# Kernel optimization log

Measured on AMD Instinct MI355X. Metric: run time of the kernel, lower is better.

Reference implementation:

```python
import jax, jax.numpy as jnp
import numpy as np

B, T, U, H, M, K, C = 64, 800, 80, 512, 20, 10, 80  # batch, tsteps, char len, rnn_size, nmixtures, kmixtures, char_vec_len


def _lstm(x, W, Uw, b):
    """Keras-semantics LSTM (gate order i,f,g,o), zero initial state. x: [B,T,D] -> [B,T,H]."""
    xg = jnp.einsum('btd,dh->bth', x, W) + b  # precompute input contribution
    h0 = jnp.zeros((x.shape[0], Uw.shape[0]), x.dtype)
    c0 = jnp.zeros_like(h0)

    def step(carry, zt):
        h, c = carry
        z = zt + h @ Uw
        i, f, g, o = jnp.split(z, 4, axis=-1)
        c = jax.nn.sigmoid(f) * c + jax.nn.sigmoid(i) * jnp.tanh(g)
        h = jax.nn.sigmoid(o) * jnp.tanh(c)
        return (h, c), h

    _, hs = jax.lax.scan(step, (h0, c0), jnp.swapaxes(xg, 0, 1))
    return jnp.swapaxes(hs, 0, 1)


def _forward(stroke_data, char_seq, kappa0, W0, U0, b0, W1, U1, b1, W2, U2, b2, Wa, ba, Wm, bm):
    lstm0_out = _lstm(stroke_data, W0, U0, b0)  # [B,T,H]
    # Attention window: the per-timestep loop in the source only carries kappa,
    # which is a running sum of exp(kappa_offset) -> vectorize via cumsum.
    abk = jnp.exp(jnp.einsum('bth,hk->btk', lstm0_out, Wa) + ba)  # [B,T,3K]
    alpha, beta, koff = jnpp_split = jnp.split(abk, 3, axis=-1)
    kappa = kappa0[:, None, :, 0] + jnp.cumsum(koff, axis=1)  # [B,T,K]
    u = jnp.arange(char_seq.shape[1], dtype=stroke_data.dtype)  # [U]
    # phi: [B,T,U] = sum_k alpha * exp(-beta * (kappa - u)^2)
    phi = jnp.sum(alpha[..., None] * jnp.exp(-beta[..., None] * (kappa[..., None] - u) ** 2), axis=2)
    windows = jnp.einsum('btu,buc->btc', phi, char_seq)  # [B,T,C]
    aug = jnp.concatenate([lstm0_out, windows, stroke_data], axis=-1)
    lstm1_out = _lstm(aug, W1, U1, b1)
    lstm2_out = _lstm(lstm1_out, W2, U2, b2)
    mdn = jnp.einsum('bth,hn->btn', lstm2_out, Wm) + bm  # [B,T,1+6M]
    eos_hat = mdn[..., 0:1]
    pi_hat, mu1, mu2, s1_hat, s2_hat, rho_hat = jnp.split(mdn[..., 1:], 6, axis=-1)
    return jnp.concatenate([
        jax.nn.sigmoid(-eos_hat),
        jax.nn.softmax(pi_hat, axis=-1),
        mu1, mu2,
        jnp.exp(s1_hat), jnp.exp(s2_hat),
        jnp.tanh(rho_hat),
    ], axis=-1)  # [B,T,1+6M]


def setup_inputs() -> dict:
    key = jax.random.key(0)
    ks = jax.random.split(key, 12)
    init = lambda k, shape: jax.random.truncated_normal(k, -2.0, 2.0, shape, jnp.float32) * 0.075
    return {
        'stroke_data': jax.random.normal(ks[0], (B, T, 3), jnp.float32),
        'char_seq': jax.nn.one_hot(jax.random.randint(ks[1], (B, U), 0, C), C, dtype=jnp.float32),
        'kappa0': jnp.zeros((B, K, 1), jnp.float32),
        'W0': init(ks[2], (3, 4 * H)), 'U0': init(ks[3], (H, 4 * H)), 'b0': jnp.zeros((4 * H,)),
        'W1': init(ks[4], (H + C + 3, 4 * H)), 'U1': init(ks[5], (H, 4 * H)), 'b1': jnp.zeros((4 * H,)),
        'W2': init(ks[6], (H, 4 * H)), 'U2': init(ks[7], (H, 4 * H)), 'b2': jnp.zeros((4 * H,)),
        'Wa': init(ks[8], (H, 3 * K)),
        'ba': -3.0 + 0.25 * jax.random.truncated_normal(ks[9], -2.0, 2.0, (3 * K,), jnp.float32),
        'Wm': init(ks[10], (H, 1 + 6 * M)), 'bm': jnp.zeros((1 + 6 * M,)),
    }


def reference(stroke_data, char_seq, kappa0, W0, U0, b0, W1, U1, b1, W2, U2, b2, Wa, ba, Wm, bm):
    return _forward(stroke_data, char_seq, kappa0, W0, U0, b0, W1, U1, b1, W2, U2, b2, Wa, ba, Wm, bm)
```

## Files before the change

### kernel.cpp

```cpp
#include <hip/hip_runtime.h>

typedef unsigned short u16;
typedef unsigned int u32;
typedef short v8s __attribute__((ext_vector_type(8)));
typedef float v4f __attribute__((ext_vector_type(4)));
typedef unsigned int v4u __attribute__((ext_vector_type(4)));
typedef unsigned int v2u __attribute__((ext_vector_type(2)));

#define MFMA16 __builtin_amdgcn_mfma_f32_16x16x32_bf16

constexpr int TT = 800;
constexpr int NBLK = 178;

constexpr int AUGB  = 2240;
constexpr int AUG2B = 2048;

constexpr size_t AUGR_OFF  = 131072;
constexpr size_t AUG2R_OFF = AUGR_OFF + (size_t)4 * 64 * AUGB;
constexpr size_t WAT_OFF   = AUG2R_OFF + (size_t)4 * 64 * AUG2B;
constexpr size_t WS_ZERO   = WAT_OFF + (size_t)32 * 512 * 2;

constexpr u32 SMEM_BYTES = 82944;

enum { G_S0D = 0, G_SAD = 1, G_S1D = 2, G_S2D = 3, G_S1R = 4, G_SAR = 5, G_S2R = 6, G_SMR = 7 };

__device__ __forceinline__ float bf2f(u16 u) { return __uint_as_float(((u32)u) << 16); }
__device__ __forceinline__ u16 f2bf(float f) {
    u32 x = __float_as_uint(f);
    return (u16)((x + 0x7fffu + ((x >> 16) & 1u)) >> 16);
}
__device__ __forceinline__ short f2bfs(float f) { return (short)f2bf(f); }
__device__ __forceinline__ float sigf(float x) { return 1.f / (1.f + __expf(-x)); }
__device__ __forceinline__ float tanhf2(float x) { return 1.f - 2.f / (1.f + __expf(2.f * x)); }

__device__ __forceinline__ __amdgpu_buffer_rsrc_t mkrsrc(const void* p) {
    return __builtin_amdgcn_make_buffer_rsrc((void*)p, (short)0, -1, 0x00020000);
}
__device__ __forceinline__ v4u ldu4(__amdgpu_buffer_rsrc_t r, int off) {
    return __builtin_amdgcn_raw_buffer_load_b128(r, off, 0, 17);
}
__device__ __forceinline__ v2u ldu8(__amdgpu_buffer_rsrc_t r, int off) {
    return __builtin_amdgcn_raw_buffer_load_b64(r, off, 0, 17);
}
__device__ __forceinline__ void stq8(__amdgpu_buffer_rsrc_t r, int off, u16 a, u16 b, u16 c, u16 d) {
    v2u t; t[0] = (u32)a | ((u32)b << 16); t[1] = (u32)c | ((u32)d << 16);
    __builtin_amdgcn_raw_buffer_store_b64(t, r, off, 0, 17);
}
__device__ __forceinline__ void stq4(__amdgpu_buffer_rsrc_t r, int off, u16 a, u16 b) {
    u32 t = (u32)a | ((u32)b << 16);
    __builtin_amdgcn_raw_buffer_store_b32(t, r, off, 0, 17);
}

__device__ __forceinline__ void publish(u32* ctrl, int g, int t, int sub) {
    __hip_atomic_fetch_add(ctrl + g * 4096 + (t & 3) * 1024 + (sub & 15) * 64, 1u,
                           __ATOMIC_RELAXED, __HIP_MEMORY_SCOPE_AGENT);
}
__device__ __forceinline__ void wait4(u32* ctrl,
    int g0, int t0, u32 n0, int m0, int g1, int t1, u32 n1, int m1,
    int g2, int t2, u32 n2, int m2, int g3, int t3, u32 n3, int m3)
{
    if (threadIdx.x < 64) {
        const int lane = threadIdx.x;
        const int cl = lane >> 4, k = lane & 15;
        int g, tt, mb; u32 nn;
        if (cl == 0)      { g = g0; tt = t0; nn = n0; mb = m0; }
        else if (cl == 1) { g = g1; tt = t1; nn = n1; mb = m1; }
        else if (cl == 2) { g = g2; tt = t2; nn = n2; mb = m2; }
        else              { g = g3; tt = t3; nn = n3; mb = m3; }
        const u32 tgt = (g >= 0 && tt >= 0) ? nn * (u32)((tt >> 2) + 1) : 0u;
        u32* p = (tgt > 0) ? (ctrl + g * 4096 + (tt & 3) * 1024 + (mb + (k & 7)) * 64) : (u32*)0;
        int sp = 0;
        for (;;) {
            u32 v = p ? __hip_atomic_load(p, __ATOMIC_RELAXED, __HIP_MEMORY_SCOPE_AGENT) : 0u;
            v += __shfl_xor(v, 1); v += __shfl_xor(v, 2);
            v += __shfl_xor(v, 4); v += __shfl_xor(v, 8);
            const bool bad = (tgt > 0) && (v < tgt);
            if (__ballot(bad) == 0ull) break;
            if (sp >= 2) __builtin_amdgcn_s_sleep(4);
            else if (sp == 1) __builtin_amdgcn_s_sleep(1);
            sp++;
        }
    }
    __syncthreads();
}

__global__ void wat_init(const float* __restrict__ Wa, u16* __restrict__ WaT) {
    __amdgpu_buffer_rsrc_t r = mkrsrc(WaT);
    for (int idx = blockIdx.x * 256 + threadIdx.x; idx < 32 * 512 / 2; idx += gridDim.x * 256) {
        const int e0 = idx * 2, e1 = e0 + 1;
        const int n0 = e0 >> 9, k0 = e0 & 511;
        const int n1 = e1 >> 9, k1 = e1 & 511;
        const u16 a = (n0 < 30) ? f2bf(Wa[k0 * 30 + n0]) : (u16)0;
        const u16 b = (n1 < 30) ? f2bf(Wa[k1 * 30 + n1]) : (u16)0;
        stq4(r, idx * 4, a, b);
    }
}

__global__ __launch_bounds__(256, 1) void hw_main(
    const float* __restrict__ stroke, const float* __restrict__ charseq, const float* __restrict__ kappa0,
    const float* __restrict__ W0, const float* __restrict__ U0, const float* __restrict__ b0,
    const float* __restrict__ W1, const float* __restrict__ U1, const float* __restrict__ b1,
    const float* __restrict__ W2, const float* __restrict__ U2, const float* __restrict__ b2,
    const float* __restrict__ ba, const float* __restrict__ Wm, const float* __restrict__ bm,
    float* __restrict__ out, char* __restrict__ ws)
{
    extern __shared__ __align__(16) char smem[];
    u32* ctrl = (u32*)ws;
    u16* augr  = (u16*)(ws + AUGR_OFF);
    u16* aug2r = (u16*)(ws + AUG2R_OFF);
    const u16* WaT = (const u16*)(ws + WAT_OFF);

    const int blk = blockIdx.x, tid = threadIdx.x;
    const int wave = tid >> 6, lane = tid & 63;
    const int quad = lane >> 4, l15 = lane & 15;

    if (blk < 32) {
        const int cs = blk & 15, mg = blk >> 4;
        const int mb = mg * 8, sub = mb + (cs & 7);
        __amdgpu_buffer_rsrc_t ra = mkrsrc(augr);
        u16*   aL  = (u16*)smem;
        float* zb  = (float*)(smem + 33280);
        float* w0s = (float*)(smem + 50176);
        float* b0s = (float*)(smem + 51712);
        if (tid < 128) {
            const int cn2 = (tid >> 5) * 512 + cs * 32 + (tid & 31);
            b0s[tid] = b0[cn2];
            #pragma unroll
            for (int d = 0; d < 3; d++) w0s[d * 128 + tid] = W0[d * 2048 + cn2];
        }
        v8s bw0[16], bw1[16];
        {
            const int cnA = wave * 512 + cs * 32 + l15;
            const int cnB = cnA + 16;
            #pragma unroll
            for (int kc = 0; kc < 16; kc++)
                #pragma unroll
                for (int j = 0; j < 8; j++) {
                    const int k = kc * 32 + quad * 8 + j;
                    bw0[kc][j] = f2bfs(U0[k * 2048 + cnA]);
                    bw1[kc][j] = f2bfs(U0[k * 2048 + cnB]);
                }
        }
        float cst[4] = {0.f, 0.f, 0.f, 0.f};
        const int bl_ = tid & 31;
        const int bpre = mg * 32 + bl_;
        __syncthreads();
        #pragma unroll 1
        for (int t = 0; t < TT; t++) {
            const float xx0 = stroke[(bpre * TT + t) * 3 + 0];
            const float xx1 = stroke[(bpre * TT + t) * 3 + 1];
            const float xx2 = stroke[(bpre * TT + t) * 3 + 2];
            wait4(ctrl, G_S0D, t - 1, 32, mb, G_S1R, t - 4, 64, mb, G_SAR, t - 4, 16, mb, -1, 0, 0, 0);
            {
                const int base = (((t + 3) & 3) * 64 + mg * 32) * AUGB;
                #pragma unroll
                for (int c8 = 0; c8 < 8; c8++) {
                    const int c = tid + 256 * c8;
                    const int row = c >> 6, off = c & 63;
                    v4u d = ldu4(ra, base + row * AUGB + off * 16);
                    *(v4u*)((char*)aL + row * 1040 + off * 16) = d;
                }
            }
            __syncthreads();
            v4f c0a = {0,0,0,0}, c0b = {0,0,0,0}, c1a = {0,0,0,0}, c1b = {0,0,0,0};
            const int xo = quad * 16;
            #pragma unroll
            for (int kc = 0; kc < 16; kc++) {
                v8s x0 = *(const v8s*)((const char*)aL + l15 * 1040 + kc * 64 + xo);
                v8s x1 = *(const v8s*)((const char*)aL + (16 + l15) * 1040 + kc * 64 + xo);
                c0a = MFMA16(x0, bw0[kc], c0a, 0, 0, 0);
                c1a = MFMA16(x0, bw1[kc], c1a, 0, 0, 0);
                c0b = MFMA16(x1, bw0[kc], c0b, 0, 0, 0);
                c1b = MFMA16(x1, bw1[kc], c1b, 0, 0, 0);
            }
            const int n0 = wave * 32 + l15, n1 = n0 + 16;
            #pragma unroll
            for (int r = 0; r < 4; r++) {
                zb[(quad * 4 + r) * 132 + n0] = c0a[r];
                zb[(quad * 4 + r) * 132 + n1] = c1a[r];
                zb[(16 + quad * 4 + r) * 132 + n0] = c0b[r];
                zb[(16 + quad * 4 + r) * 132 + n1] = c1b[r];
            }
            __syncthreads();
            {
                const int bl = tid & 31, jj = tid >> 5;
                const int b = mg * 32 + bl;
                u16 hv[4];
                #pragma unroll
                for (int m = 0; m < 4; m++) {
                    const int j = jj * 4 + m;
                    float z[4];
                    #pragma unroll
                    for (int g = 0; g < 4; g++) {
                        const int n = g * 32 + j;
                        z[g] = zb[bl * 132 + n] + b0s[n] + xx0 * w0s[n] + xx1 * w0s[128 + n] + xx2 * w0s[256 + n];
                    }
                    const float cc = sigf(z[1]) * cst[m] + sigf(z[0]) * tanhf2(z[2]);
                    cst[m] = cc;
                    hv[m] = f2bf(sigf(z[3]) * tanhf2(cc));
                }
                stq8(ra, ((t & 3) * 64 + b) * AUGB + (cs * 32 + jj * 4) * 2, hv[0], hv[1], hv[2], hv[3]);
            }
            __syncthreads();
            if (tid == 0) publish(ctrl, G_S0D, t, sub);
        }
    } else if (blk < 96) {
        const int q = blk - 32, cs = q >> 1, mg = q & 1;
        const int mb = mg * 8, sub = mb + (cs & 7);
        __amdgpu_buffer_rsrc_t ra = mkrsrc(augr);
        __amdgpu_buffer_rsrc_t r2 = mkrsrc(aug2r);
        u16*   aL  = (u16*)smem;
        float* zb  = (float*)(smem + 72192);
        float* b1s = (float*)(smem + 80896);
        if (tid < 64) b1s[tid] = b1[(tid >> 4) * 512 + cs * 16 + (tid & 15)];
        v8s bw[35];
        {
            const int cn = wave * 512 + cs * 16 + l15;
            #pragma unroll
            for (int kc = 0; kc < 35; kc++)
                #pragma unroll
                for (int j = 0; j < 8; j++) {
                    const int k = kc * 32 + quad * 8 + j;
                    short v = 0;
                    if (k < 595) v = f2bfs(W1[k * 2048 + cn]);
                    else if (k >= 596 && k < 1108) v = f2bfs(U1[(k - 596) * 2048 + cn]);
                    bw[kc][j] = v;
                }
        }
        if (tid < 32) { v4u z4 = {0,0,0,0}; *(v4u*)((char*)aL + tid * 2256 + 2224) = z4; }
        float cst[2] = {0.f, 0.f};
        __syncthreads();
        #pragma unroll 1
        for (int t = 0; t < TT; t++) {
            wait4(ctrl, G_S0D, t, 32, mb, G_SAD, t, 16, mb, G_S2R, t - 4, 64, mb, -1, 0, 0, 0);
            {
                const int base = ((t & 3) * 64 + mg * 32) * AUGB;
                #pragma unroll
                for (int c10 = 0; c10 < 10; c10++) {
                    const int c = tid + 256 * c10;
                    if (c < 2400) {
                        const int row = c / 75, off = c - row * 75;
                        v4u d = ldu4(ra, base + row * AUGB + off * 16);
                        *(v4u*)((char*)aL + row * 2256 + off * 16) = d;
                    }
                }
            }
            __syncthreads();
            if (tid == 0) publish(ctrl, G_S1R, t, sub);
            wait4(ctrl, G_S1D, t - 1, 64, mb, -1, 0, 0, 0, -1, 0, 0, 0, -1, 0, 0, 0);
            {
                const int base = ((t & 3) * 64 + mg * 32) * AUGB;
                if (tid < 32) {
                    v2u d8 = ldu8(ra, base + tid * AUGB + 1192);
                    *(v2u*)((char*)aL + tid * 2256 + 1192) = d8;
                }
                #pragma unroll
                for (int c8 = 0; c8 < 8; c8++) {
                    const int c = tid + 256 * c8;
                    const int row = c >> 6, off = 75 + (c & 63);
                    v4u d = ldu4(ra, base + row * AUGB + off * 16);
                    *(v4u*)((char*)aL + row * 2256 + off * 16) = d;
                }
            }
            v4f c0 = {0,0,0,0}, c1 = {0,0,0,0};
            const int xo = quad * 16;
            #pragma unroll
            for (int kc = 0; kc < 18; kc++) {
                v8s x0 = *(const v8s*)((const char*)aL + l15 * 2256 + kc * 64 + xo);
                v8s x1 = *(const v8s*)((const char*)aL + (16 + l15) * 2256 + kc * 64 + xo);
                c0 = MFMA16(x0, bw[kc], c0, 0, 0, 0);
                c1 = MFMA16(x1, bw[kc], c1, 0, 0, 0);
            }
            __syncthreads();
            #pragma unroll
            for (int kc = 18; kc < 35; kc++) {
                v8s x0 = *(const v8s*)((const char*)aL + l15 * 2256 + kc * 64 + xo);
                v8s x1 = *(const v8s*)((const char*)aL + (16 + l15) * 2256 + kc * 64 + xo);
                c0 = MFMA16(x0, bw[kc], c0, 0, 0, 0);
                c1 = MFMA16(x1, bw[kc], c1, 0, 0, 0);
            }
            #pragma unroll
            for (int r = 0; r < 4; r++) {
                zb[(quad * 4 + r) * 68 + wave * 17 + l15] = c0[r];
                zb[(16 + quad * 4 + r) * 68 + wave * 17 + l15] = c1[r];
            }
            __syncthreads();
            {
                const int bl = tid & 31, jj = tid >> 5;
                const int b = mg * 32 + bl;
                u16 hv[2];
                #pragma unroll
                for (int m = 0; m < 2; m++) {
                    const int j = jj * 2 + m;
                    float z[4];
                    #pragma unroll
                    for (int g = 0; g < 4; g++)
                        z[g] = zb[bl * 68 + g * 17 + j] + b1s[g * 16 + j];
                    const float cc = sigf(z[1]) * cst[m] + sigf(z[0]) * tanhf2(z[2]);
                    cst[m] = cc;
                    hv[m] = f2bf(sigf(z[3]) * tanhf2(cc));
                }
                stq4(ra, (((t + 1) & 3) * 64 + b) * AUGB + (596 + cs * 16 + jj * 2) * 2, hv[0], hv[1]);
                stq4(r2, ((t & 3) * 64 + b) * AUG2B + (cs * 16 + jj * 2) * 2, hv[0], hv[1]);
            }
            __syncthreads();
            if (tid == 0) publish(ctrl, G_S1D, t, sub);
        }
    } else if (blk < 160) {
        const int q = blk - 96, cs = q >> 1, mg = q & 1;
        const int mb = mg * 8, sub = mb + (cs & 7);
        __amdgpu_buffer_rsrc_t r2 = mkrsrc(aug2r);
        u16*   aL  = (u16*)smem;
        float* zb  = (float*)(smem + 66048);
        float* b2s = (float*)(smem + 74752);
        if (tid < 64) b2s[tid] = b2[(tid >> 4) * 512 + cs * 16 + (tid & 15)];
        v8s bw[32];
        {
            const int cn = wave * 512 + cs * 16 + l15;
            #pragma unroll
            for (int kc = 0; kc < 32; kc++)
                #pragma unroll
                for (int j = 0; j < 8; j++) {
                    const int k = kc * 32 + quad * 8 + j;
                    bw[kc][j] = (k < 512) ? f2bfs(W2[k * 2048 + cn]) : f2bfs(U2[(k - 512) * 2048 + cn]);
                }
        }
        float cst[2] = {0.f, 0.f};
        __syncthreads();
        #pragma unroll 1
        for (int t = 0; t < TT; t++) {
            wait4(ctrl, G_S1D, t, 64, mb, G_SMR, t - 4, 2, mb, -1, 0, 0, 0, -1, 0, 0, 0);
            {
                const int base = ((t & 3) * 64 + mg * 32) * AUG2B;
                #pragma unroll
                for (int c8 = 0; c8 < 8; c8++) {
                    const int c = tid + 256 * c8;
                    const int row = c >> 6, off = c & 63;
                    v4u d = ldu4(r2, base + row * AUG2B + off * 16);
                    *(v4u*)((char*)aL + row * 2064 + off * 16) = d;
                }
            }
            __syncthreads();
            if (tid == 0) publish(ctrl, G_S2R, t, sub);
            wait4(ctrl, G_S2D, t - 1, 64, mb, -1, 0, 0, 0, -1, 0, 0, 0, -1, 0, 0, 0);
            {
                const int base = ((t & 3) * 64 + mg * 32) * AUG2B;
                #pragma unroll
                for (int c8 = 0; c8 < 8; c8++) {
                    const int c = tid + 256 * c8;
                    const int row = c >> 6, off = 64 + (c & 63);
                    v4u d = ldu4(r2, base + row * AUG2B + off * 16);
                    *(v4u*)((char*)aL + row * 2064 + off * 16) = d;
                }
            }
            v4f c0 = {0,0,0,0}, c1 = {0,0,0,0};
            const int xo = quad * 16;
            #pragma unroll
            for (int kc = 0; kc < 16; kc++) {
                v8s x0 = *(const v8s*)((const char*)aL + l15 * 2064 + kc * 64 + xo);
                v8s x1 = *(const v8s*)((const char*)aL + (16 + l15) * 2064 + kc * 64 + xo);
                c0 = MFMA16(x0, bw[kc], c0, 0, 0, 0);
                c1 = MFMA16(x1, bw[kc], c1, 0, 0, 0);
            }
            __syncthreads();
            #pragma unroll
            for (int kc = 16; kc < 32; kc++) {
                v8s x0 = *(const v8s*)((const char*)aL + l15 * 2064 + kc * 64 + xo);
                v8s x1 = *(const v8s*)((const char*)aL + (16 + l15) * 2064 + kc * 64 + xo);
                c0 = MFMA16(x0, bw[kc], c0, 0, 0, 0);
                c1 = MFMA16(x1, bw[kc], c1, 0, 0, 0);
            }
            #pragma unroll
            for (int r = 0; r < 4; r++) {
                zb[(quad * 4 + r) * 68 + wave * 17 + l15] = c0[r];
                zb[(16 + quad * 4 + r) * 68 + wave * 17 + l15] = c1[r];
            }
            __syncthreads();
            {
                const int bl = tid & 31, jj = tid >> 5;
                const int b = mg * 32 + bl;
                u16 hv[2];
                #pragma unroll
                for (int m = 0; m < 2; m++) {
                    const int j = jj * 2 + m;
                    float z[4];
                    #pragma unroll
                    for (int g = 0; g < 4; g++)
                        z[g] = zb[bl * 68 + g * 17 + j] + b2s[g * 16 + j];
                    const float cc = sigf(z[1]) * cst[m] + sigf(z[0]) * tanhf2(z[2]);
                    cst[m] = cc;
                    hv[m] = f2bf(sigf(z[3]) * tanhf2(cc));
                }
                stq4(r2, (((t + 1) & 3) * 64 + b) * AUG2B + (512 + cs * 16 + jj * 2) * 2, hv[0], hv[1]);
            }
            __syncthreads();
            if (tid == 0) publish(ctrl, G_S2D, t, sub);
        }
    } else if (blk < 176) {
        const int a = blk - 160;
        const int mg = a >> 3, mb = mg * 8, sub = mb + (a & 7);
        const int b = a * 4 + wave;
        __amdgpu_buffer_rsrc_t ra = mkrsrc(augr);
        u16*   watl = (u16*)smem;
        u16*   hrow = (u16*)(smem + 33280);
        float* phis = (float*)(smem + 37440);
        u16*   idxs = (u16*)(smem + 38720);
        {
            #pragma unroll
            for (int c8 = 0; c8 < 8; c8++) {
                const int c = tid + 256 * c8;
                const int row = c >> 6, off = c & 63;
                *(v4u*)((char*)watl + row * 1040 + off * 16) = *(const v4u*)(WaT + row * 512 + off * 8);
            }
        }
        #pragma unroll
        for (int rep = 0; rep < 2; rep++) {
            const int u = rep * 64 + lane;
            if (u < 80) {
                int c = 0;
                #pragma unroll 1
                for (int cc = 0; cc < 80; cc++)
                    if (charseq[b * 6400 + u * 80 + cc] > 0.5f) c = cc;
                idxs[wave * 80 + u] = (u16)c;
            }
        }
        float kap = (lane < 10) ? kappa0[b * 10 + lane] : 0.f;
        const float baf = (lane < 30) ? ba[lane] : 0.f;
        const int nn = lane & 31;
        const int k0 = (lane >> 5) * 256;
        const u16* wrow = watl + nn * 520 + k0;
        __syncthreads();
        #pragma unroll 1
        for (int t = 0; t < TT; t++) {
            float sx0 = 0.f, sx1 = 0.f;
            if (lane == 40) { sx0 = stroke[(b * TT + t) * 3 + 0]; sx1 = stroke[(b * TT + t) * 3 + 1]; }
            else if (lane == 41) { sx0 = stroke[(b * TT + t) * 3 + 2]; }
            wait4(ctrl, G_S0D, t, 32, mb, G_S1R, t - 4, 64, mb, -1, 0, 0, 0, -1, 0, 0, 0);
            {
                const int row = tid >> 6, off = tid & 63;
                v4u d = ldu4(ra, ((t & 3) * 64 + a * 4 + row) * AUGB + off * 16);
                *(v4u*)((char*)hrow + row * 1040 + off * 16) = d;
            }
            __syncthreads();
            if (tid == 0) publish(ctrl, G_SAR, t, sub);
            float acc = 0.f;
            #pragma unroll
            for (int kk = 0; kk < 32; kk++) {
                v8s hv = *(const v8s*)((const char*)hrow + wave * 1040 + (k0 + kk * 8) * 2);
                v8s wv = *(const v8s*)(wrow + kk * 8);
                #pragma unroll
                for (int e = 0; e < 8; e++) acc += bf2f((u16)hv[e]) * bf2f((u16)wv[e]);
            }
            acc += __shfl_xor(acc, 32);
            const float abk = __expf(acc + baf);
            const float kofv = __shfl(abk, 20 + (lane < 10 ? lane : 0));
            if (lane < 10) kap += kofv;
            const float u1f = (float)lane;
            float p1 = 0.f, p2 = 0.f;
            #pragma unroll
            for (int kk = 0; kk < 10; kk++) {
                const float al = __shfl(abk, kk);
                const float be = __shfl(abk, 10 + kk);
                const float kp = __shfl(kap, kk);
                const float d1 = kp - u1f, d2 = kp - (u1f + 64.f);
                p1 += al * __expf(-be * d1 * d1);
                p2 += al * __expf(-be * d2 * d2);
            }
            phis[wave * 80 + lane] = p1;
            if (lane < 16) phis[wave * 80 + 64 + lane] = p2;
            __syncthreads();
            const int db = (((t & 3) * 64 + b) * AUGB) + 512 * 2;
            if (lane < 40) {
                const int c0 = 2 * lane;
                float w0 = 0.f, w1 = 0.f;
                #pragma unroll 1
                for (int u = 0; u < 80; u++) {
                    const float pv = phis[wave * 80 + u];
                    const int ix = (int)idxs[wave * 80 + u];
                    w0 += (ix == c0)     ? pv : 0.f;
                    w1 += (ix == c0 + 1) ? pv : 0.f;
                }
                stq4(ra, db + c0 * 2, f2bf(w0), f2bf(w1));
            } else if (lane == 40) {
                stq4(ra, db + 80 * 2, f2bf(sx0), f2bf(sx1));
            } else if (lane == 41) {
                stq4(ra, db + 82 * 2, f2bf(sx0), (u16)0);
            }
            __syncthreads();
            if (tid == 0) publish(ctrl, G_SAD, t, sub);
        }
    } else {
        const int mgs = blk - 176;
        const int mb = mgs * 8, sub = mb;
        __amdgpu_buffer_rsrc_t r2 = mkrsrc(aug2r);
        u16*   aL = (u16*)smem;
        float* zb = (float*)(smem + 33280);
        v8s bw0[16], bw1[16];
        {
            const int nA = wave * 32 + l15, nB = nA + 16;
            #pragma unroll
            for (int kc = 0; kc < 16; kc++)
                #pragma unroll
                for (int j = 0; j < 8; j++) {
                    const int k = kc * 32 + quad * 8 + j;
                    bw0[kc][j] = (nA < 121) ? f2bfs(Wm[k * 121 + nA]) : (short)0;
                    bw1[kc][j] = (nB < 121) ? f2bfs(Wm[k * 121 + nB]) : (short)0;
                }
        }
        __syncthreads();
        #pragma unroll 1
        for (int t = 0; t < TT; t++) {
            wait4(ctrl, G_S2D, t, 64, mb, -1, 0, 0, 0, -1, 0, 0, 0, -1, 0, 0, 0);
            {
                const int base = (((t + 1) & 3) * 64 + mgs * 32) * AUG2B + 1024;
                #pragma unroll
                for (int c8 = 0; c8 < 8; c8++) {
                    const int c = tid + 256 * c8;
                    const int row = c >> 6, off = c & 63;
                    v4u d = ldu4(r2, base + row * AUG2B + off * 16);
                    *(v4u*)((char*)aL + row * 1040 + off * 16) = d;
                }
            }
            __syncthreads();
            if (tid == 0) publish(ctrl, G_SMR, t, sub);
            v4f c0a = {0,0,0,0}, c0b = {0,0,0,0}, c1a = {0,0,0,0}, c1b = {0,0,0,0};
            const int xo = quad * 16;
            #pragma unroll
            for (int kc = 0; kc < 16; kc++) {
                v8s x0 = *(const v8s*)((const char*)aL + l15 * 1040 + kc * 64 + xo);
                v8s x1 = *(const v8s*)((const char*)aL + (16 + l15) * 1040 + kc * 64 + xo);
                c0a = MFMA16(x0, bw0[kc], c0a, 0, 0, 0);
                c1a = MFMA16(x0, bw1[kc], c1a, 0, 0, 0);
                c0b = MFMA16(x1, bw0[kc], c0b, 0, 0, 0);
                c1b = MFMA16(x1, bw1[kc], c1b, 0, 0, 0);
            }
            const int n0 = wave * 32 + l15, n1 = n0 + 16;
            #pragma unroll
            for (int r = 0; r < 4; r++) {
                zb[(quad * 4 + r) * 132 + n0] = c0a[r];
                zb[(quad * 4 + r) * 132 + n1] = c1a[r];
                zb[(16 + quad * 4 + r) * 132 + n0] = c0b[r];
                zb[(16 + quad * 4 + r) * 132 + n1] = c1b[r];
            }
            __syncthreads();
            {
                const int b8 = tid >> 3, g8 = tid & 7;
                const int b = mgs * 32 + b8;
                const float* zr = zb + b8 * 132;
                float* orow = out + ((size_t)(b * TT + t)) * 121;
                if (g8 == 0) {
                    orow[0] = sigf(-(zr[0] + bm[0]));
                    float mx = -1e30f;
                    float zv[20];
                    #pragma unroll 1
                    for (int nl = 1; nl <= 20; nl++) { zv[nl - 1] = zr[nl] + bm[nl]; mx = fmaxf(mx, zv[nl - 1]); }
                    float ss = 0.f;
                    #pragma unroll 1
                    for (int nl = 0; nl < 20; nl++) { zv[nl] = __expf(zv[nl] - mx); ss += zv[nl]; }
                    const float inv = 1.f / ss;
                    #pragma unroll 1
                    for (int nl = 0; nl < 20; nl++) orow[nl + 1] = zv[nl] * inv;
                } else if (g8 <= 2) {
                    const int s0 = 21 + (g8 - 1) * 20;
                    #pragma unroll 1
                    for (int nl = s0; nl < s0 + 20; nl++) orow[nl] = zr[nl] + bm[nl];
                } else if (g8 <= 4) {
                    const int s0 = 61 + (g8 - 3) * 20;
                    #pragma unroll 1
                    for (int nl = s0; nl < s0 + 20; nl++) orow[nl] = __expf(zr[nl] + bm[nl]);
                } else if (g8 <= 6) {
                    const int s0 = 101 + (g8 - 5) * 10;
                    #pragma unroll 1
                    for (int nl = s0; nl < s0 + 10; nl++) orow[nl] = tanhf2(zr[nl] + bm[nl]);
                }
            }
            __syncthreads();
        }
    }
}

extern "C" void kernel_launch(void* const* d_in, const int* in_sizes, int n_in,
                              void* d_out, int out_size, void* d_ws, size_t ws_size,
                              hipStream_t stream) {
    const float* stroke  = (const float*)d_in[0];
    const float* charseq = (const float*)d_in[1];
    const float* kappa0  = (const float*)d_in[2];
    const float* W0 = (const float*)d_in[3];
    const float* U0 = (const float*)d_in[4];
    const float* b0 = (const float*)d_in[5];
    const float* W1 = (const float*)d_in[6];
    const float* U1 = (const float*)d_in[7];
    const float* b1 = (const float*)d_in[8];
    const float* W2 = (const float*)d_in[9];
    const float* U2 = (const float*)d_in[10];
    const float* b2 = (const float*)d_in[11];
    const float* Wa = (const float*)d_in[12];
    const float* ba = (const float*)d_in[13];
    const float* Wm = (const float*)d_in[14];
    const float* bm = (const float*)d_in[15];
    char* ws = (char*)d_ws;

    static bool attr_done = false;
    if (!attr_done) {
        hipFuncSetAttribute((const void*)hw_main,
                            hipFuncAttributeMaxDynamicSharedMemorySize, SMEM_BYTES);
        attr_done = true;
    }

    hipMemsetAsync(d_ws, 0, WS_ZERO, stream);
    wat_init<<<8, 256, 0, stream>>>(Wa, (u16*)(ws + WAT_OFF));
    hw_main<<<NBLK, 256, SMEM_BYTES, stream>>>(stroke, charseq, kappa0, W0, U0, b0,
                                               W1, U1, b1, W2, U2, b2, ba, Wm, bm,
                                               (float*)d_out, ws);
}
```

Baseline: 8.748 ms.

## Fuse attention into LSTM0 blocks and merge LSTM1/LSTM2 into skewed blocks

Removes the separate attention blocks and folds the window computation into the LSTM0 blocks, one step behind. It also fuses the LSTM1 and LSTM2 layers into the same 64 blocks using a skewed (tau, tau-1) schedule, which cuts the grid from 178 to 98 blocks and reduces the cross-block flag stages per timestep. Polling now uses buffer loads with cache-bypass bits and a shorter sleep. The cost is more registers, since each block holds both weight sets, and more shared memory per block. It also adds serial attention work on the LSTM0 critical path.

```diff
diff --git a/kernel.cpp b/kernel.cpp
--- a/kernel.cpp
+++ b/kernel.cpp
@@ -10,9 +10,9 @@
 #define MFMA16 __builtin_amdgcn_mfma_f32_16x16x32_bf16
 
 constexpr int TT = 800;
-constexpr int NBLK = 178;
-
-constexpr int AUGB  = 2240;
+constexpr int NBLK = 98;
+
+constexpr int AUGB  = 1216;
 constexpr int AUG2B = 2048;
 
 constexpr size_t AUGR_OFF  = 131072;
@@ -20,9 +20,9 @@
 constexpr size_t WAT_OFF   = AUG2R_OFF + (size_t)4 * 64 * AUG2B;
 constexpr size_t WS_ZERO   = WAT_OFF + (size_t)32 * 512 * 2;
 
-constexpr u32 SMEM_BYTES = 82944;
-
-enum { G_S0D = 0, G_SAD = 1, G_S1D = 2, G_S2D = 3, G_S1R = 4, G_SAR = 5, G_S2R = 6, G_SMR = 7 };
+constexpr u32 SMEM_BYTES = 123904;
+
+enum { G_S0D = 0, G_S12D = 1, G_S12R = 2, G_SMR = 3 };
 
 __device__ __forceinline__ float bf2f(u16 u) { return __uint_as_float(((u32)u) << 16); }
 __device__ __forceinline__ u16 f2bf(float f) {
@@ -39,9 +39,6 @@
 __device__ __forceinline__ v4u ldu4(__amdgpu_buffer_rsrc_t r, int off) {
     return __builtin_amdgcn_raw_buffer_load_b128(r, off, 0, 17);
 }
-__device__ __forceinline__ v2u ldu8(__amdgpu_buffer_rsrc_t r, int off) {
-    return __builtin_amdgcn_raw_buffer_load_b64(r, off, 0, 17);
-}
 __device__ __forceinline__ void stq8(__amdgpu_buffer_rsrc_t r, int off, u16 a, u16 b, u16 c, u16 d) {
     v2u t; t[0] = (u32)a | ((u32)b << 16); t[1] = (u32)c | ((u32)d << 16);
     __builtin_amdgcn_raw_buffer_store_b64(t, r, off, 0, 17);
@@ -49,6 +46,22 @@
 __device__ __forceinline__ void stq4(__amdgpu_buffer_rsrc_t r, int off, u16 a, u16 b) {
     u32 t = (u32)a | ((u32)b << 16);
     __builtin_amdgcn_raw_buffer_store_b32(t, r, off, 0, 17);
+}
+
+__device__ __forceinline__ v4u mksrd(const void* p) {
+    v4u r;
+    r[0] = (u32)(size_t)p;
+    r[1] = (u32)((size_t)p >> 32);
+    r[2] = 0xFFFFFFFFu;
+    r[3] = 0x00020000u;
+    return r;
+}
+__device__ __forceinline__ u32 poll_ld(v4u srd, int off) {
+    u32 v;
+    asm volatile("buffer_load_dword %0, %1, %2, 0 offen sc0 sc1\n\t"
+                 "s_waitcnt vmcnt(0)"
+                 : "=v"(v) : "v"(off), "s"(srd) : "memory");
+    return v;
 }
 
 __device__ __forceinline__ void publish(u32* ctrl, int g, int t, int sub) {
@@ -68,15 +81,16 @@
         else if (cl == 2) { g = g2; tt = t2; nn = n2; mb = m2; }
         else              { g = g3; tt = t3; nn = n3; mb = m3; }
         const u32 tgt = (g >= 0 && tt >= 0) ? nn * (u32)((tt >> 2) + 1) : 0u;
-        u32* p = (tgt > 0) ? (ctrl + g * 4096 + (tt & 3) * 1024 + (mb + (k & 7)) * 64) : (u32*)0;
+        const v4u srd = mksrd(ctrl);
+        const int boff = (g >= 0) ? (g * 4096 + ((tt & 3)) * 1024 + (mb + (k & 7)) * 64) * 4 : 0;
         int sp = 0;
         for (;;) {
-            u32 v = p ? __hip_atomic_load(p, __ATOMIC_RELAXED, __HIP_MEMORY_SCOPE_AGENT) : 0u;
+            u32 v = (tgt > 0) ? poll_ld(srd, boff) : 0u;
             v += __shfl_xor(v, 1); v += __shfl_xor(v, 2);
             v += __shfl_xor(v, 4); v += __shfl_xor(v, 8);
             const bool bad = (tgt > 0) && (v < tgt);
             if (__ballot(bad) == 0ull) break;
-            if (sp >= 2) __builtin_amdgcn_s_sleep(4);
+            if (sp >= 2) __builtin_amdgcn_s_sleep(2);
             else if (sp == 1) __builtin_amdgcn_s_sleep(1);
             sp++;
         }
@@ -118,16 +132,46 @@
         const int cs = blk & 15, mg = blk >> 4;
         const int mb = mg * 8, sub = mb + (cs & 7);
         __amdgpu_buffer_rsrc_t ra = mkrsrc(augr);
-        u16*   aL  = (u16*)smem;
-        float* zb  = (float*)(smem + 33280);
-        float* w0s = (float*)(smem + 50176);
-        float* b0s = (float*)(smem + 51712);
+        u16*   aL   = (u16*)smem;
+        float* zb   = (float*)(smem + 33280);
+        float* w0s  = (float*)(smem + 50176);
+        float* b0s  = (float*)(smem + 51712);
+        u16*   watl = (u16*)(smem + 52224);
+        float* phis = (float*)(smem + 85504);
+        u16*   idxs = (u16*)(smem + 86144);
         if (tid < 128) {
             const int cn2 = (tid >> 5) * 512 + cs * 32 + (tid & 31);
             b0s[tid] = b0[cn2];
             #pragma unroll
             for (int d = 0; d < 3; d++) w0s[d * 128 + tid] = W0[d * 2048 + cn2];
         }
+        {
+            #pragma unroll
+            for (int c8 = 0; c8 < 8; c8++) {
+                const int c = tid + 256 * c8;
+                const int row = c >> 6, off = c & 63;
+                *(v4u*)((char*)watl + row * 1040 + off * 16) = *(const v4u*)(WaT + row * 512 + off * 8);
+            }
+        }
+        const int batt = mg * 32 + 2 * cs + wave;
+        if (wave < 2) {
+            #pragma unroll
+            for (int rep = 0; rep < 2; rep++) {
+                const int u_ = rep * 64 + lane;
+                if (u_ < 80) {
+                    int c = 0;
+                    #pragma unroll 1
+                    for (int cc = 0; cc < 80; cc++)
+                        if (charseq[batt * 6400 + u_ * 80 + cc] > 0.5f) c = cc;
+                    idxs[wave * 80 + u_] = (u16)c;
+                }
+            }
+        }
+        float kap = (wave < 2 && lane < 10) ? kappa0[batt * 10 + lane] : 0.f;
+        const float baf = (lane < 30) ? ba[lane] : 0.f;
+        const int nn = lane & 31;
+        const int k0 = (lane >> 5) * 256;
+        const u16* wrow = watl + nn * 520 + k0;
         v8s bw0[16], bw1[16];
         {
             const int cnA = wave * 512 + cs * 32 + l15;
@@ -142,17 +186,24 @@
                 }
         }
         float cst[4] = {0.f, 0.f, 0.f, 0.f};
-        const int bl_ = tid & 31;
-        const int bpre = mg * 32 + bl_;
+        const int bpre = mg * 32 + (tid & 31);
         __syncthreads();
         #pragma unroll 1
-        for (int t = 0; t < TT; t++) {
-            const float xx0 = stroke[(bpre * TT + t) * 3 + 0];
-            const float xx1 = stroke[(bpre * TT + t) * 3 + 1];
-            const float xx2 = stroke[(bpre * TT + t) * 3 + 2];
-            wait4(ctrl, G_S0D, t - 1, 32, mb, G_S1R, t - 4, 64, mb, G_SAR, t - 4, 16, mb, -1, 0, 0, 0);
+        for (int u = 0; u <= TT; u++) {
+            float xx0 = 0.f, xx1 = 0.f, xx2 = 0.f;
+            if (u < TT) {
+                xx0 = stroke[(bpre * TT + u) * 3 + 0];
+                xx1 = stroke[(bpre * TT + u) * 3 + 1];
+                xx2 = stroke[(bpre * TT + u) * 3 + 2];
+            }
+            float sx0 = 0.f, sx1 = 0.f;
+            if (u >= 1 && wave < 2) {
+                if (lane == 40) { sx0 = stroke[(batt * TT + u - 1) * 3 + 0]; sx1 = stroke[(batt * TT + u - 1) * 3 + 1]; }
+                else if (lane == 41) { sx0 = stroke[(batt * TT + u - 1) * 3 + 2]; }
+            }
+            wait4(ctrl, G_S0D, u - 1, 32, mb, G_S12R, u - 4, 64, mb, -1, 0, 0, 0, -1, 0, 0, 0);
             {
-                const int base = (((t + 3) & 3) * 64 + mg * 32) * AUGB;
+                const int base = (((u + 3) & 3) * 64 + mg * 32) * AUGB;
                 #pragma unroll
                 for (int c8 = 0; c8 < 8; c8++) {
                     const int c = tid + 256 * c8;
@@ -162,27 +213,29 @@
                 }
             }
             __syncthreads();
-            v4f c0a = {0,0,0,0}, c0b = {0,0,0,0}, c1a = {0,0,0,0}, c1b = {0,0,0,0};
-            const int xo = quad * 16;
-            #pragma unroll
-            for (int kc = 0; kc < 16; kc++) {
-                v8s x0 = *(const v8s*)((const char*)aL + l15 * 1040 + kc * 64 + xo);
-                v8s x1 = *(const v8s*)((const char*)aL + (16 + l15) * 1040 + kc * 64 + xo);
-                c0a = MFMA16(x0, bw0[kc], c0a, 0, 0, 0);
-                c1a = MFMA16(x0, bw1[kc], c1a, 0, 0, 0);
-                c0b = MFMA16(x1, bw0[kc], c0b, 0, 0, 0);
-                c1b = MFMA16(x1, bw1[kc], c1b, 0, 0, 0);
-            }
-            const int n0 = wave * 32 + l15, n1 = n0 + 16;
-            #pragma unroll
-            for (int r = 0; r < 4; r++) {
-                zb[(quad * 4 + r) * 132 + n0] = c0a[r];
-                zb[(quad * 4 + r) * 132 + n1] = c1a[r];
-                zb[(16 + quad * 4 + r) * 132 + n0] = c0b[r];
-                zb[(16 + quad * 4 + r) * 132 + n1] = c1b[r];
-            }
-            __syncthreads();
-            {
+            if (u < TT) {
+                v4f c0a = {0,0,0,0}, c0b = {0,0,0,0}, c1a = {0,0,0,0}, c1b = {0,0,0,0};
+                const int xo = quad * 16;
+                #pragma unroll
+                for (int kc = 0; kc < 16; kc++) {
+                    v8s x0 = *(const v8s*)((const char*)aL + l15 * 1040 + kc * 64 + xo);
+                    v8s x1 = *(const v8s*)((const char*)aL + (16 + l15) * 1040 + kc * 64 + xo);
+                    c0a = MFMA16(x0, bw0[kc], c0a, 0, 0, 0);
+                    c1a = MFMA16(x0, bw1[kc], c1a, 0, 0, 0);
+                    c0b = MFMA16(x1, bw0[kc], c0b, 0, 0, 0);
+                    c1b = MFMA16(x1, bw1[kc], c1b, 0, 0, 0);
+                }
+                const int n0 = wave * 32 + l15, n1 = n0 + 16;
+                #pragma unroll
+                for (int r = 0; r < 4; r++) {
+                    zb[(quad * 4 + r) * 132 + n0] = c0a[r];
+                    zb[(quad * 4 + r) * 132 + n1] = c1a[r];
+                    zb[(16 + quad * 4 + r) * 132 + n0] = c0b[r];
+                    zb[(16 + quad * 4 + r) * 132 + n1] = c1b[r];
+                }
+            }
+            __syncthreads();
+            if (u < TT) {
                 const int bl = tid & 31, jj = tid >> 5;
                 const int b = mg * 32 + bl;
                 u16 hv[4];
@@ -199,21 +252,77 @@
                     cst[m] = cc;
                     hv[m] = f2bf(sigf(z[3]) * tanhf2(cc));
                 }
-                stq8(ra, ((t & 3) * 64 + b) * AUGB + (cs * 32 + jj * 4) * 2, hv[0], hv[1], hv[2], hv[3]);
-            }
-            __syncthreads();
-            if (tid == 0) publish(ctrl, G_S0D, t, sub);
+                stq8(ra, ((u & 3) * 64 + b) * AUGB + (cs * 32 + jj * 4) * 2, hv[0], hv[1], hv[2], hv[3]);
+            }
+            if (u >= 1) {
+                if (wave < 2) {
+                    float acc = 0.f;
+                    #pragma unroll
+                    for (int kk = 0; kk < 32; kk++) {
+                        v8s hv = *(const v8s*)((const char*)aL + (2 * cs + wave) * 1040 + (k0 + kk * 8) * 2);
+                        v8s wv = *(const v8s*)(wrow + kk * 8);
+                        #pragma unroll
+                        for (int e = 0; e < 8; e++) acc += bf2f((u16)hv[e]) * bf2f((u16)wv[e]);
+                    }
+                    acc += __shfl_xor(acc, 32);
+                    const float abk = __expf(acc + baf);
+                    const float kofv = __shfl(abk, 20 + (lane < 10 ? lane : 0));
+                    if (lane < 10) kap += kofv;
+                    const float u1f = (float)lane;
+                    float p1 = 0.f, p2 = 0.f;
+                    #pragma unroll
+                    for (int kk = 0; kk < 10; kk++) {
+                        const float al = __shfl(abk, kk);
+                        const float be = __shfl(abk, 10 + kk);
+                        const float kp = __shfl(kap, kk);
+                        const float d1 = kp - u1f, d2 = kp - (u1f + 64.f);
+                        p1 += al * __expf(-be * d1 * d1);
+                        p2 += al * __expf(-be * d2 * d2);
+                    }
+                    phis[wave * 80 + lane] = p1;
+                    if (lane < 16) phis[wave * 80 + 64 + lane] = p2;
+                }
+                __syncthreads();
+                if (wave < 2) {
+                    const int db = ((((u - 1) & 3) * 64 + batt) * AUGB) + 512 * 2;
+                    if (lane < 40) {
+                        const int c0 = 2 * lane;
+                        float w0 = 0.f, w1 = 0.f;
+                        #pragma unroll 1
+                        for (int uu = 0; uu < 80; uu++) {
+                            const float pv = phis[wave * 80 + uu];
+                            const int ix = (int)idxs[wave * 80 + uu];
+                            w0 += (ix == c0)     ? pv : 0.f;
+                            w1 += (ix == c0 + 1) ? pv : 0.f;
+                        }
+                        stq4(ra, db + c0 * 2, f2bf(w0), f2bf(w1));
+                    } else if (lane == 40) {
+                        stq4(ra, db + 80 * 2, f2bf(sx0), f2bf(sx1));
+                    } else if (lane == 41) {
+                        stq4(ra, db + 82 * 2, f2bf(sx0), (u16)0);
+                    }
+                }
+            }
+            __syncthreads();
+            if (tid == 0) publish(ctrl, G_S0D, u, sub);
         }
     } else if (blk < 96) {
         const int q = blk - 32, cs = q >> 1, mg = q & 1;
         const int mb = mg * 8, sub = mb + (cs & 7);
         __amdgpu_buffer_rsrc_t ra = mkrsrc(augr);
         __amdgpu_buffer_rsrc_t r2 = mkrsrc(aug2r);
-        u16*   aL  = (u16*)smem;
-        float* zb  = (float*)(smem + 72192);
-        float* b1s = (float*)(smem + 80896);
-        if (tid < 64) b1s[tid] = b1[(tid >> 4) * 512 + cs * 16 + (tid & 15)];
-        v8s bw[35];
+        u16*   aLa = (u16*)smem;
+        u16*   aLb = (u16*)(smem + 39424);
+        u16*   aLc = (u16*)(smem + 72704);
+        float* zb1 = (float*)(smem + 105984);
+        float* zb2 = (float*)(smem + 114688);
+        float* b1s = (float*)(smem + 123392);
+        float* b2s = (float*)(smem + 123648);
+        if (tid < 64) {
+            b1s[tid] = b1[(tid >> 4) * 512 + cs * 16 + (tid & 15)];
+            b2s[tid] = b2[(tid >> 4) * 512 + cs * 16 + (tid & 15)];
+        }
+        v8s bw1[35], bw2[32];
         {
             const int cn = wave * 512 + cs * 16 + l15;
             #pragma unroll
@@ -222,276 +331,128 @@
                 for (int j = 0; j < 8; j++) {
                     const int k = kc * 32 + quad * 8 + j;
                     short v = 0;
-                    if (k < 595) v = f2bfs(W1[k * 2048 + cn]);
-                    else if (k >= 596 && k < 1108) v = f2bfs(U1[(k - 596) * 2048 + cn]);
-                    bw[kc][j] = v;
-                }
-        }
-        if (tid < 32) { v4u z4 = {0,0,0,0}; *(v4u*)((char*)aL + tid * 2256 + 2224) = z4; }
-        float cst[2] = {0.f, 0.f};
+                    if (kc < 19) { if (k < 595) v = f2bfs(W1[k * 2048 + cn]); }
+                    else v = f2bfs(U1[(k - 608) * 2048 + cn]);
+                    bw1[kc][j] = v;
+                }
+            #pragma unroll
+            for (int kc = 0; kc < 32; kc++)
+                #pragma unroll
+                for (int j = 0; j < 8; j++) {
+                    const int k = kc * 32 + quad * 8 + j;
+                    bw2[kc][j] = (kc < 16) ? f2bfs(W2[k * 2048 + cn]) : f2bfs(U2[(k - 512) * 2048 + cn]);
+                }
+        }
+        float cst1[2] = {0.f, 0.f}, cst2[2] = {0.f, 0.f};
         __syncthreads();
         #pragma unroll 1
-        for (int t = 0; t < TT; t++) {
-            wait4(ctrl, G_S0D, t, 32, mb, G_SAD, t, 16, mb, G_S2R, t - 4, 64, mb, -1, 0, 0, 0);
+        for (int tau = 0; tau <= TT; tau++) {
+            const int s0t = (tau < TT) ? tau + 1 : TT;
+            wait4(ctrl, G_S0D, s0t, 32, mb, G_S12D, tau - 1, 64, mb, G_SMR, tau - 4, 2, mb, -1, 0, 0, 0);
             {
-                const int base = ((t & 3) * 64 + mg * 32) * AUGB;
+                const int base_a = ((tau & 3) * 64 + mg * 32) * AUGB;
+                const int base_b = (((tau + 3) & 3) * 64 + mg * 32) * AUG2B;
+                const int base_c = (((tau + 2) & 3) * 64 + mg * 32) * AUG2B + 1024;
                 #pragma unroll
                 for (int c10 = 0; c10 < 10; c10++) {
                     const int c = tid + 256 * c10;
-                    if (c < 2400) {
-                        const int row = c / 75, off = c - row * 75;
-                        v4u d = ldu4(ra, base + row * AUGB + off * 16);
-                        *(v4u*)((char*)aL + row * 2256 + off * 16) = d;
-                    }
-                }
-            }
-            __syncthreads();
-            if (tid == 0) publish(ctrl, G_S1R, t, sub);
-            wait4(ctrl, G_S1D, t - 1, 64, mb, -1, 0, 0, 0, -1, 0, 0, 0, -1, 0, 0, 0);
-            {
-                const int base = ((t & 3) * 64 + mg * 32) * AUGB;
-                if (tid < 32) {
-                    v2u d8 = ldu8(ra, base + tid * AUGB + 1192);
-                    *(v2u*)((char*)aL + tid * 2256 + 1192) = d8;
+                    if (c < 2432) {
+                        const int row = c / 76, off = c - row * 76;
+                        v4u d = ldu4(ra, base_a + row * AUGB + off * 16);
+                        *(v4u*)((char*)aLa + row * 1232 + off * 16) = d;
+                    }
                 }
                 #pragma unroll
                 for (int c8 = 0; c8 < 8; c8++) {
                     const int c = tid + 256 * c8;
-                    const int row = c >> 6, off = 75 + (c & 63);
-                    v4u d = ldu4(ra, base + row * AUGB + off * 16);
-                    *(v4u*)((char*)aL + row * 2256 + off * 16) = d;
-                }
-            }
+                    const int row = c >> 6, off = c & 63;
+                    v4u d = ldu4(r2, base_b + row * AUG2B + off * 16);
+                    *(v4u*)((char*)aLb + row * 1040 + off * 16) = d;
+                }
+                #pragma unroll
+                for (int c8 = 0; c8 < 8; c8++) {
+                    const int c = tid + 256 * c8;
+                    const int row = c >> 6, off = c & 63;
+                    v4u d = ldu4(r2, base_c + row * AUG2B + off * 16);
+                    *(v4u*)((char*)aLc + row * 1040 + off * 16) = d;
+                }
+            }
+            __syncthreads();
+            if (tid == 0) publish(ctrl, G_S12R, tau, sub);
             v4f c0 = {0,0,0,0}, c1 = {0,0,0,0};
+            v4f d0 = {0,0,0,0}, d1 = {0,0,0,0};
             const int xo = quad * 16;
             #pragma unroll
-            for (int kc = 0; kc < 18; kc++) {
-                v8s x0 = *(const v8s*)((const char*)aL + l15 * 2256 + kc * 64 + xo);
-                v8s x1 = *(const v8s*)((const char*)aL + (16 + l15) * 2256 + kc * 64 + xo);
-                c0 = MFMA16(x0, bw[kc], c0, 0, 0, 0);
-                c1 = MFMA16(x1, bw[kc], c1, 0, 0, 0);
-            }
-            __syncthreads();
-            #pragma unroll
-            for (int kc = 18; kc < 35; kc++) {
-                v8s x0 = *(const v8s*)((const char*)aL + l15 * 2256 + kc * 64 + xo);
-                v8s x1 = *(const v8s*)((const char*)aL + (16 + l15) * 2256 + kc * 64 + xo);
-                c0 = MFMA16(x0, bw[kc], c0, 0, 0, 0);
-                c1 = MFMA16(x1, bw[kc], c1, 0, 0, 0);
+            for (int kc = 0; kc < 16; kc++) {
+                v8s x0 = *(const v8s*)((const char*)aLb + l15 * 1040 + kc * 64 + xo);
+                v8s x1 = *(const v8s*)((const char*)aLb + (16 + l15) * 1040 + kc * 64 + xo);
+                c0 = MFMA16(x0, bw1[19 + kc], c0, 0, 0, 0);
+                d0 = MFMA16(x0, bw2[kc], d0, 0, 0, 0);
+                c1 = MFMA16(x1, bw1[19 + kc], c1, 0, 0, 0);
+                d1 = MFMA16(x1, bw2[kc], d1, 0, 0, 0);
+            }
+            #pragma unroll
+            for (int kc = 0; kc < 19; kc++) {
+                v8s y0 = *(const v8s*)((const char*)aLa + l15 * 1232 + kc * 64 + xo);
+                v8s y1 = *(const v8s*)((const char*)aLa + (16 + l15) * 1232 + kc * 64 + xo);
+                c0 = MFMA16(y0, bw1[kc], c0, 0, 0, 0);
+                c1 = MFMA16(y1, bw1[kc], c1, 0, 0, 0);
+            }
+            #pragma unroll
+            for (int kc = 0; kc < 16; kc++) {
+                v8s z0 = *(const v8s*)((const char*)aLc + l15 * 1040 + kc * 64 + xo);
+                v8s z1 = *(const v8s*)((const char*)aLc + (16 + l15) * 1040 + kc * 64 + xo);
+                d0 = MFMA16(z0, bw2[16 + kc], d0, 0, 0, 0);
+                d1 = MFMA16(z1, bw2[16 + kc], d1, 0, 0, 0);
             }
             #pragma unroll
             for (int r = 0; r < 4; r++) {
-                zb[(quad * 4 + r) * 68 + wave * 17 + l15] = c0[r];
-                zb[(16 + quad * 4 + r) * 68 + wave * 17 + l15] = c1[r];
+                zb1[(quad * 4 + r) * 68 + wave * 17 + l15] = c0[r];
+                zb1[(16 + quad * 4 + r) * 68 + wave * 17 + l15] = c1[r];
+                zb2[(quad * 4 + r) * 68 + wave * 17 + l15] = d0[r];
+                zb2[(16 + quad * 4 + r) * 68 + wave * 17 + l15] = d1[r];
             }
             __syncthreads();
             {
                 const int bl = tid & 31, jj = tid >> 5;
                 const int b = mg * 32 + bl;
-                u16 hv[2];
-                #pragma unroll
-                for (int m = 0; m < 2; m++) {
-                    const int j = jj * 2 + m;
-                    float z[4];
+                if (tau < TT) {
+                    u16 hv[2];
                     #pragma unroll
-                    for (int g = 0; g < 4; g++)
-                        z[g] = zb[bl * 68 + g * 17 + j] + b1s[g * 16 + j];
-                    const float cc = sigf(z[1]) * cst[m] + sigf(z[0]) * tanhf2(z[2]);
-                    cst[m] = cc;
-                    hv[m] = f2bf(sigf(z[3]) * tanhf2(cc));
-                }
-                stq4(ra, (((t + 1) & 3) * 64 + b) * AUGB + (596 + cs * 16 + jj * 2) * 2, hv[0], hv[1]);
-                stq4(r2, ((t & 3) * 64 + b) * AUG2B + (cs * 16 + jj * 2) * 2, hv[0], hv[1]);
-            }
-            __syncthreads();
-            if (tid == 0) publish(ctrl, G_S1D, t, sub);
-        }
-    } else if (blk < 160) {
-        const int q = blk - 96, cs = q >> 1, mg = q & 1;
-        const int mb = mg * 8, sub = mb + (cs & 7);
-        __amdgpu_buffer_rsrc_t r2 = mkrsrc(aug2r);
-        u16*   aL  = (u16*)smem;
-        float* zb  = (float*)(smem + 66048);
-        float* b2s = (float*)(smem + 74752);
-        if (tid < 64) b2s[tid] = b2[(tid >> 4) * 512 + cs * 16 + (tid & 15)];
-        v8s bw[32];
-        {
-            const int cn = wave * 512 + cs * 16 + l15;
-            #pragma unroll
-            for (int kc = 0; kc < 32; kc++)
-                #pragma unroll
-                for (int j = 0; j < 8; j++) {
-                    const int k = kc * 32 + quad * 8 + j;
-                    bw[kc][j] = (k < 512) ? f2bfs(W2[k * 2048 + cn]) : f2bfs(U2[(k - 512) * 2048 + cn]);
-                }
-        }
-        float cst[2] = {0.f, 0.f};
-        __syncthreads();
-        #pragma unroll 1
-        for (int t = 0; t < TT; t++) {
-            wait4(ctrl, G_S1D, t, 64, mb, G_SMR, t - 4, 2, mb, -1, 0, 0, 0, -1, 0, 0, 0);
-            {
-                const int base = ((t & 3) * 64 + mg * 32) * AUG2B;
-                #pragma unroll
-                for (int c8 = 0; c8 < 8; c8++) {
-                    const int c = tid + 256 * c8;
-                    const int row = c >> 6, off = c & 63;
-                    v4u d = ldu4(r2, base + row * AUG2B + off * 16);
-                    *(v4u*)((char*)aL + row * 2064 + off * 16) = d;
-                }
-            }
-            __syncthreads();
-            if (tid == 0) publish(ctrl, G_S2R, t, sub);
-            wait4(ctrl, G_S2D, t - 1, 64, mb, -1, 0, 0, 0, -1, 0, 0, 0, -1, 0, 0, 0);
-            {
-                const int base = ((t & 3) * 64 + mg * 32) * AUG2B;
-                #pragma unroll
-                for (int c8 = 0; c8 < 8; c8++) {
-                    const int c = tid + 256 * c8;
-                    const int row = c >> 6, off = 64 + (c & 63);
-                    v4u d = ldu4(r2, base + row * AUG2B + off * 16);
-                    *(v4u*)((char*)aL + row * 2064 + off * 16) = d;
-                }
-            }
-            v4f c0 = {0,0,0,0}, c1 = {0,0,0,0};
-            const int xo = quad * 16;
-            #pragma unroll
-            for (int kc = 0; kc < 16; kc++) {
-                v8s x0 = *(const v8s*)((const char*)aL + l15 * 2064 + kc * 64 + xo);
-                v8s x1 = *(const v8s*)((const char*)aL + (16 + l15) * 2064 + kc * 64 + xo);
-                c0 = MFMA16(x0, bw[kc], c0, 0, 0, 0);
-                c1 = MFMA16(x1, bw[kc], c1, 0, 0, 0);
-            }
-            __syncthreads();
-            #pragma unroll
-            for (int kc = 16; kc < 32; kc++) {
-                v8s x0 = *(const v8s*)((const char*)aL + l15 * 2064 + kc * 64 + xo);
-                v8s x1 = *(const v8s*)((const char*)aL + (16 + l15) * 2064 + kc * 64 + xo);
-                c0 = MFMA16(x0, bw[kc], c0, 0, 0, 0);
-                c1 = MFMA16(x1, bw[kc], c1, 0, 0, 0);
-            }
-            #pragma unroll
-            for (int r = 0; r < 4; r++) {
-                zb[(quad * 4 + r) * 68 + wave * 17 + l15] = c0[r];
-                zb[(16 + quad * 4 + r) * 68 + wave * 17 + l15] = c1[r];
-            }
-            __syncthreads();
-            {
-                const int bl = tid & 31, jj = tid >> 5;
-                const int b = mg * 32 + bl;
-                u16 hv[2];
-                #pragma unroll
-                for (int m = 0; m < 2; m++) {
-                    const int j = jj * 2 + m;
-                    float z[4];
+                    for (int m = 0; m < 2; m++) {
+                        const int j = jj * 2 + m;
+                        float z[4];
+                        #pragma unroll
+                        for (int g = 0; g < 4; g++)
+                            z[g] = zb1[bl * 68 + g * 17 + j] + b1s[g * 16 + j];
+                        const float cc = sigf(z[1]) * cst1[m] + sigf(z[0]) * tanhf2(z[2]);
+                        cst1[m] = cc;
+                        hv[m] = f2bf(sigf(z[3]) * tanhf2(cc));
+                    }
+                    stq4(r2, ((tau & 3) * 64 + b) * AUG2B + (cs * 16 + jj * 2) * 2, hv[0], hv[1]);
+                }
+                if (tau >= 1) {
+                    u16 hv[2];
                     #pragma unroll
-                    for (int g = 0; g < 4; g++)
-                        z[g] = zb[bl * 68 + g * 17 + j] + b2s[g * 16 + j];
-                    const float cc = sigf(z[1]) * cst[m] + sigf(z[0]) * tanhf2(z[2]);
-                    cst[m] = cc;
-                    hv[m] = f2bf(sigf(z[3]) * tanhf2(cc));
-                }
-                stq4(r2, (((t + 1) & 3) * 64 + b) * AUG2B + (512 + cs * 16 + jj * 2) * 2, hv[0], hv[1]);
-            }
-            __syncthreads();
-            if (tid == 0) publish(ctrl, G_S2D, t, sub);
-        }
-    } else if (blk < 176) {
-        const int a = blk - 160;
-        const int mg = a >> 3, mb = mg * 8, sub = mb + (a & 7);
-        const int b = a * 4 + wave;
-        __amdgpu_buffer_rsrc_t ra = mkrsrc(augr);
-        u16*   watl = (u16*)smem;
-        u16*   hrow = (u16*)(smem + 33280);
-        float* phis = (float*)(smem + 37440);
-        u16*   idxs = (u16*)(smem + 38720);
-        {
-            #pragma unroll
-            for (int c8 = 0; c8 < 8; c8++) {
-                const int c = tid + 256 * c8;
-                const int row = c >> 6, off = c & 63;
-                *(v4u*)((char*)watl + row * 1040 + off * 16) = *(const v4u*)(WaT + row * 512 + off * 8);
-            }
-        }
-        #pragma unroll
-        for (int rep = 0; rep < 2; rep++) {
-            const int u = rep * 64 + lane;
-            if (u < 80) {
-                int c = 0;
-                #pragma unroll 1
-                for (int cc = 0; cc < 80; cc++)
-                    if (charseq[b * 6400 + u * 80 + cc] > 0.5f) c = cc;
-                idxs[wave * 80 + u] = (u16)c;
-            }
-        }
-        float kap = (lane < 10) ? kappa0[b * 10 + lane] : 0.f;
-        const float baf = (lane < 30) ? ba[lane] : 0.f;
-        const int nn = lane & 31;
-        const int k0 = (lane >> 5) * 256;
-        const u16* wrow = watl + nn * 520 + k0;
-        __syncthreads();
-        #pragma unroll 1
-        for (int t = 0; t < TT; t++) {
-            float sx0 = 0.f, sx1 = 0.f;
-            if (lane == 40) { sx0 = stroke[(b * TT + t) * 3 + 0]; sx1 = stroke[(b * TT + t) * 3 + 1]; }
-            else if (lane == 41) { sx0 = stroke[(b * TT + t) * 3 + 2]; }
-            wait4(ctrl, G_S0D, t, 32, mb, G_S1R, t - 4, 64, mb, -1, 0, 0, 0, -1, 0, 0, 0);
-            {
-                const int row = tid >> 6, off = tid & 63;
-                v4u d = ldu4(ra, ((t & 3) * 64 + a * 4 + row) * AUGB + off * 16);
-                *(v4u*)((char*)hrow + row * 1040 + off * 16) = d;
-            }
-            __syncthreads();
-            if (tid == 0) publish(ctrl, G_SAR, t, sub);
-            float acc = 0.f;
-            #pragma unroll
-            for (int kk = 0; kk < 32; kk++) {
-                v8s hv = *(const v8s*)((const char*)hrow + wave * 1040 + (k0 + kk * 8) * 2);
-                v8s wv = *(const v8s*)(wrow + kk * 8);
-                #pragma unroll
-                for (int e = 0; e < 8; e++) acc += bf2f((u16)hv[e]) * bf2f((u16)wv[e]);
-            }
-            acc += __shfl_xor(acc, 32);
-            const float abk = __expf(acc + baf);
-            const float kofv = __shfl(abk, 20 + (lane < 10 ? lane : 0));
-            if (lane < 10) kap += kofv;
-            const float u1f = (float)lane;
-            float p1 = 0.f, p2 = 0.f;
-            #pragma unroll
-            for (int kk = 0; kk < 10; kk++) {
-                const float al = __shfl(abk, kk);
-                const float be = __shfl(abk, 10 + kk);
-                const float kp = __shfl(kap, kk);
-                const float d1 = kp - u1f, d2 = kp - (u1f + 64.f);
-                p1 += al * __expf(-be * d1 * d1);
-                p2 += al * __expf(-be * d2 * d2);
-            }
-            phis[wave * 80 + lane] = p1;
-            if (lane < 16) phis[wave * 80 + 64 + lane] = p2;
-            __syncthreads();
-            const int db = (((t & 3) * 64 + b) * AUGB) + 512 * 2;
-            if (lane < 40) {
-                const int c0 = 2 * lane;
-                float w0 = 0.f, w1 = 0.f;
-                #pragma unroll 1
-                for (int u = 0; u < 80; u++) {
-                    const float pv = phis[wave * 80 + u];
-                    const int ix = (int)idxs[wave * 80 + u];
-                    w0 += (ix == c0)     ? pv : 0.f;
-                    w1 += (ix == c0 + 1) ? pv : 0.f;
-                }
-                stq4(ra, db + c0 * 2, f2bf(w0), f2bf(w1));
-            } else if (lane == 40) {
-                stq4(ra, db + 80 * 2, f2bf(sx0), f2bf(sx1));
-            } else if (lane == 41) {
-                stq4(ra, db + 82 * 2, f2bf(sx0), (u16)0);
-            }
-            __syncthreads();
-            if (tid == 0) publish(ctrl, G_SAD, t, sub);
+                    for (int m = 0; m < 2; m++) {
+                        const int j = jj * 2 + m;
+                        float z[4];
+                        #pragma unroll
+                        for (int g = 0; g < 4; g++)
+                            z[g] = zb2[bl * 68 + g * 17 + j] + b2s[g * 16 + j];
+                        const float cc = sigf(z[1]) * cst2[m] + sigf(z[0]) * tanhf2(z[2]);
+                        cst2[m] = cc;
+                        hv[m] = f2bf(sigf(z[3]) * tanhf2(cc));
+                    }
+                    stq4(r2, (((tau + 3) & 3) * 64 + b) * AUG2B + 1024 + (cs * 16 + jj * 2) * 2, hv[0], hv[1]);
+                }
+            }
+            __syncthreads();
+            if (tid == 0) publish(ctrl, G_S12D, tau, sub);
         }
     } else {
-        const int mgs = blk - 176;
-        const int mb = mgs * 8, sub = mb;
+        const int mgs = blk - 96;
+        const int mb = mgs * 8;
         __amdgpu_buffer_rsrc_t r2 = mkrsrc(aug2r);
         u16*   aL = (u16*)smem;
         float* zb = (float*)(smem + 33280);
@@ -510,9 +471,9 @@
         __syncthreads();
         #pragma unroll 1
         for (int t = 0; t < TT; t++) {
-            wait4(ctrl, G_S2D, t, 64, mb, -1, 0, 0, 0, -1, 0, 0, 0, -1, 0, 0, 0);
+            wait4(ctrl, G_S12D, t + 1, 64, mb, -1, 0, 0, 0, -1, 0, 0, 0, -1, 0, 0, 0);
             {
-                const int base = (((t + 1) & 3) * 64 + mgs * 32) * AUG2B + 1024;
+                const int base = ((t & 3) * 64 + mgs * 32) * AUG2B + 1024;
                 #pragma unroll
                 for (int c8 = 0; c8 < 8; c8++) {
                     const int c = tid + 256 * c8;
@@ -522,7 +483,7 @@
                 }
             }
             __syncthreads();
-            if (tid == 0) publish(ctrl, G_SMR, t, sub);
+            if (tid == 0) publish(ctrl, G_SMR, t, mb);
             v4f c0a = {0,0,0,0}, c0b = {0,0,0,0}, c1a = {0,0,0,0}, c1b = {0,0,0,0};
             const int xo = quad * 16;
             #pragma unroll
```

Result: slower. 9.357 ms (+7.0%).
